# Performance work log

Hardware: AMD Instinct MI355X
Metric: run time of the kernel (lower is better)

Reference implementation:

```python
import jax, jax.numpy as jnp
import numpy as np

DIM = 1536
HEADS = 12
HD = DIM // HEADS  # 128
F, H, W = 4, 22, 40
L = F * H * W      # 3520
B = 1
EPS = 1e-6
SCALE = 1.0 / (HD ** 0.5)


def _rope_angles(max_pos=1024, head_dim=HD):
    # Wan rope_params: three blocks for (F,H,W) axes, dims (d-4*(d//6), 2*(d//6), 2*(d//6))
    d6 = head_dim // 6
    dims = [head_dim - 4 * d6, 2 * d6, 2 * d6]  # 44, 42, 42
    parts = []
    pos = np.arange(max_pos, dtype=np.float64)
    for dp in dims:
        inv = 1.0 / (10000.0 ** (np.arange(0, dp, 2, dtype=np.float64) / dp))
        parts.append(np.outer(pos, inv))  # [1024, dp//2]
    return np.concatenate(parts, axis=1).astype(np.float32)  # [1024, 64]


def setup_inputs() -> dict:
    key = jax.random.key(0)
    ks = jax.random.split(key, 10)
    std = 0.02
    inp = {
        "x": jax.random.normal(ks[0], (B, L, DIM), jnp.float32),
        "seq_lens": jnp.full((B,), L, jnp.int32),
        "grid_sizes": jnp.array([[F, H, W]], jnp.int32),
        "freqs": jnp.asarray(_rope_angles()),
        "Wq": jax.random.normal(ks[1], (DIM, DIM), jnp.float32) * std,
        "bq": jnp.zeros((DIM,), jnp.float32),
        "Wk": jax.random.normal(ks[2], (DIM, DIM), jnp.float32) * std,
        "bk": jnp.zeros((DIM,), jnp.float32),
        "Wv": jax.random.normal(ks[3], (DIM, DIM), jnp.float32) * std,
        "bv": jnp.zeros((DIM,), jnp.float32),
        "Wo": jax.random.normal(ks[4], (DIM, DIM), jnp.float32) * std,
        "bo": jnp.zeros((DIM,), jnp.float32),
        "gq": jnp.ones((DIM,), jnp.float32),
        "gk": jnp.ones((DIM,), jnp.float32),
    }
    return inp


def _rmsnorm(x, g):
    return x * jax.lax.rsqrt(jnp.mean(x * x, axis=-1, keepdims=True) + EPS) * g


def _rope_apply(x, grid_sizes, freqs):
    # x: [B, L, n, d]; freqs: [1024, d//2] angles. 3D grid RoPE (interleaved complex pairs).
    c = x.shape[-1] // 2  # 64
    sf = c - 2 * (c // 3)  # 22 freq channels for F axis; 21 each for H, W
    ff, fh, fw = freqs[:, :sf], freqs[:, sf:sf + c // 3], freqs[:, sf + c // 3:]

    def per_sample(xb, g):  # xb: [L, n, d], g: [3]
        f, h, w = g[0], g[1], g[2]
        idx = jnp.arange(xb.shape[0])
        fi = idx // (h * w)
        hi = (idx // w) % h
        wi = idx % w
        ang = jnp.concatenate([ff[fi], fh[hi], fw[wi]], axis=-1)  # [L, c]
        cos = jnp.cos(ang)[:, None, :]
        sin = jnp.sin(ang)[:, None, :]
        xr = xb.reshape(xb.shape[0], xb.shape[1], c, 2)
        x0, x1 = xr[..., 0], xr[..., 1]
        out = jnp.stack([x0 * cos - x1 * sin, x0 * sin + x1 * cos], axis=-1)
        return out.reshape(xb.shape)

    return jax.vmap(per_sample)(x, grid_sizes)


def reference(x, seq_lens, grid_sizes, freqs, Wq, bq, Wk, bk, Wv, bv, Wo, bo, gq, gk):
    b, s = x.shape[0], x.shape[1]
    q = _rmsnorm(x @ Wq.T + bq, gq).reshape(b, s, HEADS, HD)
    k = _rmsnorm(x @ Wk.T + bk, gk).reshape(b, s, HEADS, HD)
    v = (x @ Wv.T + bv).reshape(b, s, HEADS, HD)
    q = _rope_apply(q, grid_sizes, freqs)
    k = _rope_apply(k, grid_sizes, freqs)
    # non-causal full attention (seq_lens == L here, no padding mask needed)
    scores = jnp.einsum('bqnd,bknd->bnqk', q, k) * SCALE
    attn = jax.nn.softmax(scores, axis=-1)
    out = jnp.einsum('bnqk,bknd->bqnd', attn, v).reshape(b, s, DIM)
    return out @ Wo.T + bo
```

## Files before the change

kernel.cpp:

```cpp
#include <hip/hip_runtime.h>
#include <hip/hip_bf16.h>
#include <cstdint>

#define DIM   1536
#define HEADS 12
#define HD    128
#define LSEQ  3520
#define MPAD  3584
#define NKV   55
#define EPSF  1e-6f
#define QSCL  0.12751729198891580f

typedef __attribute__((ext_vector_type(4))) float f32x4;
typedef __attribute__((ext_vector_type(8))) short bf16x8;

__device__ __forceinline__ void gload16(const void* g, void* l) {
  __builtin_amdgcn_global_load_lds(
      (const __attribute__((address_space(1))) void*)g,
      (__attribute__((address_space(3))) void*)l, 16, 0, 0);
}

__device__ __forceinline__ ushort f2bf(float f) {
  union { float f; unsigned u; } v; v.f = f;
  unsigned u = v.u;
  return (ushort)((u + 0x7FFFu + ((u >> 16) & 1u)) >> 16);
}

__device__ __forceinline__ float bf2f(ushort u) {
  union { unsigned u; float f; } v; v.u = ((unsigned)u) << 16;
  return v.f;
}

#if __has_builtin(__builtin_amdgcn_exp2f)
__device__ __forceinline__ float ex2(float x) { return __builtin_amdgcn_exp2f(x); }
#else
__device__ __forceinline__ float ex2(float x) { return exp2f(x); }
#endif

__device__ __forceinline__ unsigned cvtpk(float a, float b) {
  unsigned r;
  asm("v_cvt_pk_bf16_f32 %0, %1, %2" : "=v"(r) : "v"(a), "v"(b));
  return r;
}

__global__ __launch_bounds__(256) void cast_all(const float* __restrict__ x,
    const float* __restrict__ Wq, const float* __restrict__ Wk,
    const float* __restrict__ Wv, const float* __restrict__ Wo,
    ushort* __restrict__ dst) {
  long e = ((long)blockIdx.x * 256 + threadIdx.x) * 8;
  const float* src;
  long off;
  if (e < (long)MPAD * DIM) {
    if (e >= (long)LSEQ * DIM) {
      *(bf16x8*)(dst + e) = (bf16x8)(short)0;
      return;
    }
    src = x; off = e;
  } else {
    long e2 = e - (long)MPAD * DIM;
    int wsel = (int)(e2 / ((long)DIM * DIM));
    off = e2 - (long)wsel * DIM * DIM;
    src = wsel == 0 ? Wq : (wsel == 1 ? Wk : (wsel == 2 ? Wv : Wo));
  }
  float4 a = *(const float4*)(src + off);
  float4 b = *(const float4*)(src + off + 4);
  bf16x8 o;
  o[0] = (short)f2bf(a.x); o[1] = (short)f2bf(a.y);
  o[2] = (short)f2bf(a.z); o[3] = (short)f2bf(a.w);
  o[4] = (short)f2bf(b.x); o[5] = (short)f2bf(b.y);
  o[6] = (short)f2bf(b.z); o[7] = (short)f2bf(b.w);
  *(bf16x8*)(dst + e) = o;
}

__global__ __launch_bounds__(256) void gemm_qkv(const ushort* __restrict__ A,
    const ushort* __restrict__ B3,
    const float* __restrict__ bq, const float* __restrict__ bk2, const float* __restrict__ bv2,
    ushort* __restrict__ qbb, ushort* __restrict__ kbb, ushort* __restrict__ vTt) {
  __shared__ ushort As[128 * 64];
  __shared__ ushort Bs[128 * 64];
  const int m0 = blockIdx.x * 128;
  const int n0g = blockIdx.y * 128;
  const int which = n0g / 1536;
  const int n0l = n0g - which * 1536;
  const int t = threadIdx.x;
  const int lane = t & 63;
  const int w = t >> 6;
  const int wr = w >> 1, wc = w & 1;
  const int sr = t >> 3;
  const int sc = t & 7;

  f32x4 acc[4][4];
#pragma unroll
  for (int i = 0; i < 4; ++i)
#pragma unroll
    for (int j = 0; j < 4; ++j) acc[i][j] = (f32x4)0.0f;

  const int arow = 64 * wr + (lane & 15);
  const int brow = 64 * wc + (lane & 15);

  for (int k0 = 0; k0 < DIM; k0 += 64) {
    __syncthreads();
#pragma unroll
    for (int i = 0; i < 4; ++i) {
      int row = sr + 32 * i;
      int cs = sc ^ (row & 7);
      gload16(A + (long)(m0 + row) * DIM + k0 + cs * 8, (char*)As + row * 128 + sc * 16);
      gload16(B3 + (long)(n0g + row) * DIM + k0 + cs * 8, (char*)Bs + row * 128 + sc * 16);
    }
    __syncthreads();
    bf16x8 af[4][2], bfr[4][2];
#pragma unroll
    for (int mi = 0; mi < 4; ++mi) {
      int row = arow + 16 * mi;
#pragma unroll
      for (int ks = 0; ks < 2; ++ks) {
        int ck = (ks * 4 + (lane >> 4)) ^ (row & 7);
        af[mi][ks] = *(const bf16x8*)(As + row * 64 + ck * 8);
      }
    }
#pragma unroll
    for (int ni = 0; ni < 4; ++ni) {
      int row = brow + 16 * ni;
#pragma unroll
      for (int ks = 0; ks < 2; ++ks) {
        int ck = (ks * 4 + (lane >> 4)) ^ (row & 7);
        bfr[ni][ks] = *(const bf16x8*)(Bs + row * 64 + ck * 8);
      }
    }
#pragma unroll
    for (int mi = 0; mi < 4; ++mi)
#pragma unroll
      for (int ni = 0; ni < 4; ++ni)
#pragma unroll
        for (int ks = 0; ks < 2; ++ks)
          acc[mi][ni] = __builtin_amdgcn_mfma_f32_16x16x32_bf16(
              af[mi][ks], bfr[ni][ks], acc[mi][ni], 0, 0, 0);
  }

  const float* bias = which == 0 ? bq : (which == 1 ? bk2 : bv2);
#pragma unroll
  for (int mi = 0; mi < 4; ++mi) {
#pragma unroll
    for (int ni = 0; ni < 4; ++ni) {
      int gmb = m0 + 64 * wr + 16 * mi + (lane >> 4) * 4;
      int gnl = n0l + 64 * wc + 16 * ni + (lane & 15);
      float bvv = bias[gnl];
      if (which == 2) {
        if (gmb < LSEQ) {
          ushort4 o;
          o.x = f2bf(acc[mi][ni][0] + bvv);
          o.y = f2bf(acc[mi][ni][1] + bvv);
          o.z = f2bf(acc[mi][ni][2] + bvv);
          o.w = f2bf(acc[mi][ni][3] + bvv);
          *(ushort4*)(vTt + (long)gnl * LSEQ + gmb) = o;
        }
      } else {
        ushort* dst = which ? kbb : qbb;
        if (gmb < LSEQ) {
#pragma unroll
          for (int j = 0; j < 4; ++j)
            dst[(long)(gmb + j) * DIM + gnl] = f2bf(acc[mi][ni][j] + bvv);
        }
      }
    }
  }
}

__global__ __launch_bounds__(256) void gemm_out(const ushort* __restrict__ A,
    const ushort* __restrict__ B, const float* __restrict__ bias,
    float* __restrict__ Cf) {
  __shared__ ushort As[128 * 64];
  __shared__ ushort Bs[128 * 64];
  const int m0 = blockIdx.x * 128;
  const int n0 = blockIdx.y * 128;
  const int t = threadIdx.x;
  const int lane = t & 63;
  const int w = t >> 6;
  const int wr = w >> 1, wc = w & 1;
  const int sr = t >> 3;
  const int sc = t & 7;

  f32x4 acc[4][4];
#pragma unroll
  for (int i = 0; i < 4; ++i)
#pragma unroll
    for (int j = 0; j < 4; ++j) acc[i][j] = (f32x4)0.0f;

  const int arow = 64 * wr + (lane & 15);
  const int brow = 64 * wc + (lane & 15);

  for (int k0 = 0; k0 < DIM; k0 += 64) {
    __syncthreads();
#pragma unroll
    for (int i = 0; i < 4; ++i) {
      int row = sr + 32 * i;
      int cs = sc ^ (row & 7);
      gload16(A + (long)(m0 + row) * DIM + k0 + cs * 8, (char*)As + row * 128 + sc * 16);
      gload16(B + (long)(n0 + row) * DIM + k0 + cs * 8, (char*)Bs + row * 128 + sc * 16);
    }
    __syncthreads();
    bf16x8 af[4][2], bfr[4][2];
#pragma unroll
    for (int mi = 0; mi < 4; ++mi) {
      int row = arow + 16 * mi;
#pragma unroll
      for (int ks = 0; ks < 2; ++ks) {
        int ck = (ks * 4 + (lane >> 4)) ^ (row & 7);
        af[mi][ks] = *(const bf16x8*)(As + row * 64 + ck * 8);
      }
    }
#pragma unroll
    for (int ni = 0; ni < 4; ++ni) {
      int row = brow + 16 * ni;
#pragma unroll
      for (int ks = 0; ks < 2; ++ks) {
        int ck = (ks * 4 + (lane >> 4)) ^ (row & 7);
        bfr[ni][ks] = *(const bf16x8*)(Bs + row * 64 + ck * 8);
      }
    }
#pragma unroll
    for (int mi = 0; mi < 4; ++mi)
#pragma unroll
      for (int ni = 0; ni < 4; ++ni)
#pragma unroll
        for (int ks = 0; ks < 2; ++ks)
          acc[mi][ni] = __builtin_amdgcn_mfma_f32_16x16x32_bf16(
              af[mi][ks], bfr[ni][ks], acc[mi][ni], 0, 0, 0);
  }

#pragma unroll
  for (int mi = 0; mi < 4; ++mi) {
#pragma unroll
    for (int ni = 0; ni < 4; ++ni) {
      int gmb = m0 + 64 * wr + 16 * mi + (lane >> 4) * 4;
      int gn  = n0 + 64 * wc + 16 * ni + (lane & 15);
      float bvv = bias[gn];
      if (gmb < LSEQ) {
#pragma unroll
        for (int j = 0; j < 4; ++j)
          Cf[(long)(gmb + j) * DIM + gn] = acc[mi][ni][j] + bvv;
      }
    }
  }
}

__global__ __launch_bounds__(256) void postqk_kernel(ushort* __restrict__ qb,
    ushort* __restrict__ kb, const float* __restrict__ gq_,
    const float* __restrict__ gk_, const float* __restrict__ freqs) {
  const int l = blockIdx.x;
  const int t = threadIdx.x;
  ushort* buf      = blockIdx.y ? kb : qb;
  const float* g   = blockIdx.y ? gk_ : gq_;
  const float post = blockIdx.y ? 1.0f : QSCL;
  ushort* row = buf + (long)l * DIM + t * 6;
  float v[6];
  {
    ushort2 p0 = *(const ushort2*)(row);
    ushort2 p1 = *(const ushort2*)(row + 2);
    ushort2 p2 = *(const ushort2*)(row + 4);
    v[0] = bf2f(p0.x); v[1] = bf2f(p0.y); v[2] = bf2f(p1.x);
    v[3] = bf2f(p1.y); v[4] = bf2f(p2.x); v[5] = bf2f(p2.y);
  }
  float ss = v[0]*v[0] + v[1]*v[1] + v[2]*v[2] + v[3]*v[3] + v[4]*v[4] + v[5]*v[5];
#pragma unroll
  for (int off = 1; off < 64; off <<= 1) ss += __shfl_xor(ss, off);
  __shared__ float red[4];
  if ((t & 63) == 0) red[t >> 6] = ss;
  __syncthreads();
  float scale = rsqrtf((red[0] + red[1] + red[2] + red[3]) * (1.0f / DIM) + EPSF) * post;
  const int fi = l / (22 * 40);
  const int hi = (l / 40) % 22;
  const int wi = l % 40;
  ushort o[6];
#pragma unroll
  for (int ii = 0; ii < 3; ++ii) {
    int pg = t * 3 + ii;
    int c = pg & 63;
    int rsel = (c < 22) ? fi : ((c < 43) ? hi : wi);
    float ang = freqs[rsel * 64 + c];
    float sn, cs;
    __sincosf(ang, &sn, &cs);
    float x0 = v[2*ii]   * scale * g[t*6 + 2*ii];
    float x1 = v[2*ii+1] * scale * g[t*6 + 2*ii+1];
    o[2*ii]   = f2bf(x0 * cs - x1 * sn);
    o[2*ii+1] = f2bf(x0 * sn + x1 * cs);
  }
  *(ushort2*)(row)     = make_ushort2(o[0], o[1]);
  *(ushort2*)(row + 2) = make_ushort2(o[2], o[3]);
  *(ushort2*)(row + 4) = make_ushort2(o[4], o[5]);
}

__global__ __launch_bounds__(256) void attn_kernel(const ushort* __restrict__ qb,
    const ushort* __restrict__ kb, const ushort* __restrict__ vT,
    ushort* __restrict__ ab) {
  __shared__ ushort KV[2][2][8192];
  __shared__ ushort Ps[4][32 * 40];
  __shared__ float2 Msh[4][2][16];
  const int qt = blockIdx.x;
  const int h  = blockIdx.y;
  const int t = threadIdx.x;
  const int lane = t & 63;
  const int w = t >> 6;
  const int a = w >> 1;
  const int b = w & 1;
  const int q16 = lane & 15;
  const int hi = lane >> 4;

  auto stageKV = [&](int buf, int kv0) {
    int rr = t >> 4, ck = t & 15;
#pragma unroll
    for (int i = 0; i < 4; ++i) {
      int row = rr + 16 * i;
      int cs = ck ^ (row & 7);
      gload16(kb + (long)(kv0 + row) * DIM + h * HD + cs * 8,
              (char*)&KV[buf][0][0] + row * 256 + ck * 16);
    }
    int rv = t >> 3, cv = t & 7;
#pragma unroll
    for (int i = 0; i < 4; ++i) {
      int row = rv + 32 * i;
      int cs = cv ^ (row & 7);
      gload16(vT + (long)(h * HD + row) * LSEQ + kv0 + cs * 8,
              (char*)&KV[buf][1][0] + row * 128 + cv * 16);
    }
  };

  {
    int rr = t >> 4, ck = t & 15;
#pragma unroll
    for (int i = 0; i < 4; ++i) {
      int row = rr + 16 * i;
      int cs = ck ^ (row & 7);
      gload16(qb + (long)(qt * 64 + row) * DIM + h * HD + cs * 8,
              (char*)&KV[1][0][0] + row * 256 + ck * 16);
    }
  }
  stageKV(0, 0);
  asm volatile("s_waitcnt vmcnt(8)" ::: "memory");
  __builtin_amdgcn_s_barrier();

  bf16x8 aq[2][4];
#pragma unroll
  for (int qf = 0; qf < 2; ++qf) {
    int row = a * 32 + qf * 16 + q16;
#pragma unroll
    for (int ks = 0; ks < 4; ++ks) {
      int ck = (ks * 4 + hi) ^ (row & 7);
      aq[qf][ks] = *(const bf16x8*)((const char*)&KV[1][0][0] + row * 256 + ck * 16);
    }
  }
  asm volatile("s_waitcnt lgkmcnt(0)" ::: "memory");
  __builtin_amdgcn_s_barrier();

  f32x4 acc[8][2];
#pragma unroll
  for (int i = 0; i < 8; ++i) { acc[i][0] = (f32x4)0.0f; acc[i][1] = (f32x4)0.0f; }
  float m_r[2] = {-1e30f, -1e30f};
  float l_r[2] = {0.f, 0.f};
  ushort* Psw = &Ps[w][0];

  auto compute = [&](int buf) {
    const ushort* Ks = &KV[buf][0][0];
    const ushort* Vs = &KV[buf][1][0];
    f32x4 s[2][2];
    s[0][0] = (f32x4)0.0f; s[0][1] = (f32x4)0.0f;
    s[1][0] = (f32x4)0.0f; s[1][1] = (f32x4)0.0f;
    __builtin_amdgcn_s_setprio(1);
#pragma unroll
    for (int kf = 0; kf < 2; ++kf) {
      int krow = b * 32 + kf * 16 + q16;
#pragma unroll
      for (int ks = 0; ks < 4; ++ks) {
        int ck = (ks * 4 + hi) ^ (krow & 7);
        bf16x8 kk = *(const bf16x8*)(Ks + krow * 128 + ck * 8);
        s[kf][0] = __builtin_amdgcn_mfma_f32_16x16x32_bf16(kk, aq[0][ks], s[kf][0], 0, 0, 0);
        s[kf][1] = __builtin_amdgcn_mfma_f32_16x16x32_bf16(kk, aq[1][ks], s[kf][1], 0, 0, 0);
      }
    }
    __builtin_amdgcn_s_setprio(0);
    float mx[2];
#pragma unroll
    for (int qf = 0; qf < 2; ++qf) {
      float m01 = fmaxf(fmaxf(s[0][qf][0], s[0][qf][1]), s[0][qf][2]);
      m01 = fmaxf(fmaxf(m01, s[0][qf][3]), s[1][qf][0]);
      m01 = fmaxf(fmaxf(m01, s[1][qf][1]), s[1][qf][2]);
      m01 = fmaxf(m01, s[1][qf][3]);
      m01 = fmaxf(m01, __shfl_xor(m01, 16));
      mx[qf] = fmaxf(m01, __shfl_xor(m01, 32));
    }
    bool noskip = !__all((mx[0] <= m_r[0] + 8.0f) & (mx[1] <= m_r[1] + 8.0f));
    if (noskip) {
#pragma unroll
      for (int qf = 0; qf < 2; ++qf) {
        float mnew = fmaxf(m_r[qf], mx[qf]);
        float fj = ex2(m_r[qf] - mnew);
        l_r[qf] *= fj;
        m_r[qf] = mnew;
#pragma unroll
        for (int ni = 0; ni < 8; ++ni) acc[ni][qf] *= fj;
      }
    }
#pragma unroll
    for (int qf = 0; qf < 2; ++qf) {
      float rs = 0.0f;
#pragma unroll
      for (int kf = 0; kf < 2; ++kf) {
        float p0 = ex2(s[kf][qf][0] - m_r[qf]);
        float p1 = ex2(s[kf][qf][1] - m_r[qf]);
        float p2 = ex2(s[kf][qf][2] - m_r[qf]);
        float p3 = ex2(s[kf][qf][3] - m_r[qf]);
        rs += (p0 + p1) + (p2 + p3);
        uint2 u;
        u.x = cvtpk(p0, p1);
        u.y = cvtpk(p2, p3);
        *(uint2*)(&Psw[(qf * 16 + q16) * 40 + kf * 16 + hi * 4]) = u;
      }
      rs += __shfl_xor(rs, 16);
      rs += __shfl_xor(rs, 32);
      l_r[qf] += rs;
    }
    bf16x8 pf[2];
    pf[0] = *(const bf16x8*)(&Psw[(0 * 16 + q16) * 40 + hi * 8]);
    pf[1] = *(const bf16x8*)(&Psw[(1 * 16 + q16) * 40 + hi * 8]);
    __builtin_amdgcn_s_setprio(1);
#pragma unroll
    for (int ni = 0; ni < 8; ++ni) {
      int vrow = 16 * ni + q16;
      int ck = (4 * b + hi) ^ (vrow & 7);
      bf16x8 vv = *(const bf16x8*)(Vs + vrow * 64 + ck * 8);
      acc[ni][0] = __builtin_amdgcn_mfma_f32_16x16x32_bf16(vv, pf[0], acc[ni][0], 0, 0, 0);
      acc[ni][1] = __builtin_amdgcn_mfma_f32_16x16x32_bf16(vv, pf[1], acc[ni][1], 0, 0, 0);
    }
    __builtin_amdgcn_s_setprio(0);
  };

  for (int tt = 0; tt < NKV - 1; ++tt) {
    stageKV((tt + 1) & 1, (tt + 1) * 64);
    asm volatile("s_waitcnt vmcnt(8)" ::: "memory");
    __builtin_amdgcn_s_barrier();
    compute(tt & 1);
    __builtin_amdgcn_s_barrier();
  }
  asm volatile("s_waitcnt vmcnt(0)" ::: "memory");
  __builtin_amdgcn_s_barrier();
  compute((NKV - 1) & 1);

  __syncthreads();
  if (hi < 2) Msh[w][hi][q16] = make_float2(m_r[hi], l_r[hi]);
  __syncthreads();
  float invl[2], fown[2];
#pragma unroll
  for (int qf = 0; qf < 2; ++qf) {
    float2 pm = Msh[w ^ 1][qf][q16];
    float ms = fmaxf(m_r[qf], pm.x);
    fown[qf] = ex2(m_r[qf] - ms);
    float ls = l_r[qf] * fown[qf] + pm.y * ex2(pm.x - ms);
    invl[qf] = 1.0f / ls;
  }
#pragma unroll
  for (int ni = 0; ni < 8; ++ni) {
    acc[ni][0] *= fown[0];
    acc[ni][1] *= fown[1];
  }
  char* xch = (char*)&KV[0][0][0] + a * 17408 + lane * 272;
  if (b == 1) {
#pragma unroll
    for (int ni = 0; ni < 8; ++ni) {
      *(f32x4*)(xch + (ni * 2 + 0) * 16) = acc[ni][0];
      *(f32x4*)(xch + (ni * 2 + 1) * 16) = acc[ni][1];
    }
  }
  __syncthreads();
  if (b == 0) {
#pragma unroll
    for (int ni = 0; ni < 8; ++ni) {
#pragma unroll
      for (int qf = 0; qf < 2; ++qf) {
        f32x4 o = acc[ni][qf] + *(const f32x4*)(xch + (ni * 2 + qf) * 16);
        float il = invl[qf];
        uint2 pk;
        pk.x = cvtpk(o[0] * il, o[1] * il);
        pk.y = cvtpk(o[2] * il, o[3] * il);
        int qrow = qt * 64 + a * 32 + qf * 16 + q16;
        *(uint2*)(ab + (long)qrow * DIM + h * HD + 16 * ni + hi * 4) = pk;
      }
    }
  }
}

extern "C" void kernel_launch(void* const* d_in, const int* in_sizes, int n_in,
                              void* d_out, int out_size, void* d_ws, size_t ws_size,
                              hipStream_t stream) {
  const float* x     = (const float*)d_in[0];
  const float* freqs = (const float*)d_in[3];
  const float* Wq = (const float*)d_in[4];  const float* bq = (const float*)d_in[5];
  const float* Wk = (const float*)d_in[6];  const float* bk = (const float*)d_in[7];
  const float* Wv = (const float*)d_in[8];  const float* bv = (const float*)d_in[9];
  const float* Wo = (const float*)d_in[10]; const float* bo = (const float*)d_in[11];
  const float* gq = (const float*)d_in[12]; const float* gk = (const float*)d_in[13];

  char* ws = (char*)d_ws;
  size_t off = 0;
  auto alloc = [&](size_t bytes) -> char* {
    char* p = ws + off;
    off += (bytes + 255) & ~(size_t)255;
    return p;
  };
  ushort* xb   = (ushort*)alloc((size_t)MPAD * DIM * 2 + 4 * (size_t)DIM * DIM * 2);
  ushort* wall = xb + (size_t)MPAD * DIM;
  ushort* wob  = wall + 3 * (size_t)DIM * DIM;
  ushort* qbb = (ushort*)alloc((size_t)LSEQ * DIM * 2);
  ushort* kbb = (ushort*)alloc((size_t)LSEQ * DIM * 2);
  ushort* vT  = (ushort*)alloc((size_t)DIM * LSEQ * 2);
  ushort* ab  = (ushort*)alloc((size_t)MPAD * DIM * 2);

  const long tot8 = ((long)MPAD * DIM + 4L * DIM * DIM) / 8;
  cast_all<<<(int)(tot8 / 256), 256, 0, stream>>>(x, Wq, Wk, Wv, Wo, xb);

  gemm_qkv<<<dim3(MPAD / 128, 36), 256, 0, stream>>>(xb, wall, bq, bk, bv, qbb, kbb, vT);

  postqk_kernel<<<dim3(LSEQ, 2), 256, 0, stream>>>(qbb, kbb, gq, gk, freqs);

  attn_kernel<<<dim3(NKV, HEADS), 256, 0, stream>>>(qbb, kbb, vT, ab);

  gemm_out<<<dim3(MPAD / 128, DIM / 128), 256, 0, stream>>>(ab, wob, bo, (float*)d_out);
}
```

Baseline: 403.4 us.

## Load V directly into registers, halve attention LDS, remap blocks per XCD

Attention no longer stages V tiles through shared memory. Each wave loads its V fragments straight from global memory into registers, which halves the LDS footprint so launch_bounds can ask for 3 blocks per CU. Blocks are launched on a 1D grid and remapped so each XCD gets a contiguous range of (head, q-tile) work, aiming for better L2 reuse of K/V per head. The epilogue exchange buffer gets an XOR swizzle to cut bank conflicts. In exchange, V global loads are uncoalesced 16-byte gathers issued inside the loop, which adds register pressure and latency.

```diff
diff --git a/kernel.cpp b/kernel.cpp
--- a/kernel.cpp
+++ b/kernel.cpp
@@ -290,14 +290,17 @@
   *(ushort2*)(row + 4) = make_ushort2(o[4], o[5]);
 }
 
-__global__ __launch_bounds__(256) void attn_kernel(const ushort* __restrict__ qb,
+__global__ __launch_bounds__(256, 3) void attn_kernel(const ushort* __restrict__ qb,
     const ushort* __restrict__ kb, const ushort* __restrict__ vT,
     ushort* __restrict__ ab) {
-  __shared__ ushort KV[2][2][8192];
+  __shared__ ushort Kd[2][64 * 128];
   __shared__ ushort Ps[4][32 * 40];
   __shared__ float2 Msh[4][2][16];
-  const int qt = blockIdx.x;
-  const int h  = blockIdx.y;
+  const int d = blockIdx.x;
+  const int xcd = d & 7, idx = d >> 3;
+  const int wflat = (xcd < 4 ? xcd * 83 : 332 + (xcd - 4) * 82) + idx;
+  const int h  = wflat / 55;
+  const int qt = wflat - h * 55;
   const int t = threadIdx.x;
   const int lane = t & 63;
   const int w = t >> 6;
@@ -306,22 +309,14 @@
   const int q16 = lane & 15;
   const int hi = lane >> 4;
 
-  auto stageKV = [&](int buf, int kv0) {
+  auto stageK = [&](int buf, int kv0) {
     int rr = t >> 4, ck = t & 15;
 #pragma unroll
     for (int i = 0; i < 4; ++i) {
       int row = rr + 16 * i;
       int cs = ck ^ (row & 7);
       gload16(kb + (long)(kv0 + row) * DIM + h * HD + cs * 8,
-              (char*)&KV[buf][0][0] + row * 256 + ck * 16);
-    }
-    int rv = t >> 3, cv = t & 7;
-#pragma unroll
-    for (int i = 0; i < 4; ++i) {
-      int row = rv + 32 * i;
-      int cs = cv ^ (row & 7);
-      gload16(vT + (long)(h * HD + row) * LSEQ + kv0 + cs * 8,
-              (char*)&KV[buf][1][0] + row * 128 + cv * 16);
+              (char*)&Kd[buf][0] + row * 256 + ck * 16);
     }
   };
 
@@ -332,11 +327,11 @@
       int row = rr + 16 * i;
       int cs = ck ^ (row & 7);
       gload16(qb + (long)(qt * 64 + row) * DIM + h * HD + cs * 8,
-              (char*)&KV[1][0][0] + row * 256 + ck * 16);
-    }
-  }
-  stageKV(0, 0);
-  asm volatile("s_waitcnt vmcnt(8)" ::: "memory");
+              (char*)&Kd[1][0] + row * 256 + ck * 16);
+    }
+  }
+  stageK(0, 0);
+  asm volatile("s_waitcnt vmcnt(4)" ::: "memory");
   __builtin_amdgcn_s_barrier();
 
   bf16x8 aq[2][4];
@@ -346,10 +341,11 @@
 #pragma unroll
     for (int ks = 0; ks < 4; ++ks) {
       int ck = (ks * 4 + hi) ^ (row & 7);
-      aq[qf][ks] = *(const bf16x8*)((const char*)&KV[1][0][0] + row * 256 + ck * 16);
+      aq[qf][ks] = *(const bf16x8*)((const char*)&Kd[1][0] + row * 256 + ck * 16);
     }
   }
   asm volatile("s_waitcnt lgkmcnt(0)" ::: "memory");
+  __builtin_amdgcn_sched_barrier(0);
   __builtin_amdgcn_s_barrier();
 
   f32x4 acc[8][2];
@@ -358,10 +354,18 @@
   float m_r[2] = {-1e30f, -1e30f};
   float l_r[2] = {0.f, 0.f};
   ushort* Psw = &Ps[w][0];
+  bf16x8 vv[8];
+
+  auto loadV = [&](int kv0) {
+#pragma unroll
+    for (int ni = 0; ni < 8; ++ni) {
+      int vrow = 16 * ni + q16;
+      vv[ni] = *(const bf16x8*)(vT + (long)(h * HD + vrow) * LSEQ + kv0 + b * 32 + hi * 8);
+    }
+  };
 
   auto compute = [&](int buf) {
-    const ushort* Ks = &KV[buf][0][0];
-    const ushort* Vs = &KV[buf][1][0];
+    const ushort* Ks = &Kd[buf][0];
     f32x4 s[2][2];
     s[0][0] = (f32x4)0.0f; s[0][1] = (f32x4)0.0f;
     s[1][0] = (f32x4)0.0f; s[1][1] = (f32x4)0.0f;
@@ -425,23 +429,22 @@
     __builtin_amdgcn_s_setprio(1);
 #pragma unroll
     for (int ni = 0; ni < 8; ++ni) {
-      int vrow = 16 * ni + q16;
-      int ck = (4 * b + hi) ^ (vrow & 7);
-      bf16x8 vv = *(const bf16x8*)(Vs + vrow * 64 + ck * 8);
-      acc[ni][0] = __builtin_amdgcn_mfma_f32_16x16x32_bf16(vv, pf[0], acc[ni][0], 0, 0, 0);
-      acc[ni][1] = __builtin_amdgcn_mfma_f32_16x16x32_bf16(vv, pf[1], acc[ni][1], 0, 0, 0);
+      acc[ni][0] = __builtin_amdgcn_mfma_f32_16x16x32_bf16(vv[ni], pf[0], acc[ni][0], 0, 0, 0);
+      acc[ni][1] = __builtin_amdgcn_mfma_f32_16x16x32_bf16(vv[ni], pf[1], acc[ni][1], 0, 0, 0);
     }
     __builtin_amdgcn_s_setprio(0);
   };
 
   for (int tt = 0; tt < NKV - 1; ++tt) {
-    stageKV((tt + 1) & 1, (tt + 1) * 64);
-    asm volatile("s_waitcnt vmcnt(8)" ::: "memory");
+    stageK((tt + 1) & 1, (tt + 1) * 64);
+    loadV(tt * 64);
+    asm volatile("s_waitcnt vmcnt(12)" ::: "memory");
     __builtin_amdgcn_s_barrier();
     compute(tt & 1);
     __builtin_amdgcn_s_barrier();
   }
-  asm volatile("s_waitcnt vmcnt(0)" ::: "memory");
+  loadV((NKV - 1) * 64);
+  asm volatile("s_waitcnt vmcnt(8)" ::: "memory");
   __builtin_amdgcn_s_barrier();
   compute((NKV - 1) & 1);
 
@@ -462,13 +465,13 @@
     acc[ni][0] *= fown[0];
     acc[ni][1] *= fown[1];
   }
-  char* xch = (char*)&KV[0][0][0] + a * 17408 + lane * 272;
+  char* xch = (char*)&Kd[0][0] + a * 16384 + lane * 256;
   if (b == 1) {
 #pragma unroll
-    for (int ni = 0; ni < 8; ++ni) {
-      *(f32x4*)(xch + (ni * 2 + 0) * 16) = acc[ni][0];
-      *(f32x4*)(xch + (ni * 2 + 1) * 16) = acc[ni][1];
-    }
+    for (int ni = 0; ni < 8; ++ni)
+#pragma unroll
+      for (int qf = 0; qf < 2; ++qf)
+        *(f32x4*)(xch + ((ni * 2 + qf) ^ (lane & 7)) * 16) = acc[ni][qf];
   }
   __syncthreads();
   if (b == 0) {
@@ -476,7 +479,7 @@
     for (int ni = 0; ni < 8; ++ni) {
 #pragma unroll
       for (int qf = 0; qf < 2; ++qf) {
-        f32x4 o = acc[ni][qf] + *(const f32x4*)(xch + (ni * 2 + qf) * 16);
+        f32x4 o = acc[ni][qf] + *(const f32x4*)(xch + ((ni * 2 + qf) ^ (lane & 7)) * 16);
         float il = invl[qf];
         uint2 pk;
         pk.x = cvtpk(o[0] * il, o[1] * il);
@@ -521,7 +524,7 @@
 
   postqk_kernel<<<dim3(LSEQ, 2), 256, 0, stream>>>(qbb, kbb, gq, gk, freqs);
 
-  attn_kernel<<<dim3(NKV, HEADS), 256, 0, stream>>>(qbb, kbb, vT, ab);
+  attn_kernel<<<NKV * HEADS, 256, 0, stream>>>(qbb, kbb, vT, ab);
 
   gemm_out<<<dim3(MPAD / 128, DIM / 128), 256, 0, stream>>>(ab, wob, bo, (float*)d_out);
 }
```

Result: slower. 541.9 us (+34.4%).

## Remap workgroup indices per XCD for L2 locality and swizzle attention exchange buffer

Applied to the files above, without the earlier changes.

Flattens the grids of the QKV GEMM, output GEMM and attention kernel, and remaps block IDs so that consecutive tiles (the same head, or neighbouring GEMM tiles) land on the same XCD, sharing that XCD's L2 for K/V and weight reuse. The attention partial-output exchange in LDS drops its padded stride in favour of an XOR swizzle to avoid bank conflicts. A sched_barrier is also added before the Q preload barrier. The mapping assumes round-robin dispatch of blocks across 8 XCDs and exact grid sizes, so it is hardcoded and brittle.

```diff
diff --git a/kernel.cpp b/kernel.cpp
--- a/kernel.cpp
+++ b/kernel.cpp
@@ -78,8 +78,11 @@
     ushort* __restrict__ qbb, ushort* __restrict__ kbb, ushort* __restrict__ vTt) {
   __shared__ ushort As[128 * 64];
   __shared__ ushort Bs[128 * 64];
-  const int m0 = blockIdx.x * 128;
-  const int n0g = blockIdx.y * 128;
+  const int dd = blockIdx.x;
+  const int f = (dd & 7) * 126 + (dd >> 3);
+  const int bx = f % 28, by = f / 28;
+  const int m0 = bx * 128;
+  const int n0g = by * 128;
   const int which = n0g / 1536;
   const int n0l = n0g - which * 1536;
   const int t = threadIdx.x;
@@ -171,8 +174,10 @@
     float* __restrict__ Cf) {
   __shared__ ushort As[128 * 64];
   __shared__ ushort Bs[128 * 64];
-  const int m0 = blockIdx.x * 128;
-  const int n0 = blockIdx.y * 128;
+  const int dd = blockIdx.x;
+  const int f = (dd & 7) * 42 + (dd >> 3);
+  const int m0 = (f % 28) * 128;
+  const int n0 = (f / 28) * 128;
   const int t = threadIdx.x;
   const int lane = t & 63;
   const int w = t >> 6;
@@ -296,8 +301,11 @@
   __shared__ ushort KV[2][2][8192];
   __shared__ ushort Ps[4][32 * 40];
   __shared__ float2 Msh[4][2][16];
-  const int qt = blockIdx.x;
-  const int h  = blockIdx.y;
+  const int d = blockIdx.x;
+  const int xcd = d & 7, idx = d >> 3;
+  const int wflat = (xcd < 4 ? xcd * 83 : 332 + (xcd - 4) * 82) + idx;
+  const int h  = wflat / 55;
+  const int qt = wflat - h * 55;
   const int t = threadIdx.x;
   const int lane = t & 63;
   const int w = t >> 6;
@@ -350,6 +358,7 @@
     }
   }
   asm volatile("s_waitcnt lgkmcnt(0)" ::: "memory");
+  __builtin_amdgcn_sched_barrier(0);
   __builtin_amdgcn_s_barrier();
 
   f32x4 acc[8][2];
@@ -462,13 +471,13 @@
     acc[ni][0] *= fown[0];
     acc[ni][1] *= fown[1];
   }
-  char* xch = (char*)&KV[0][0][0] + a * 17408 + lane * 272;
+  char* xch = (char*)&KV[0][0][0] + a * 16384 + lane * 256;
   if (b == 1) {
 #pragma unroll
-    for (int ni = 0; ni < 8; ++ni) {
-      *(f32x4*)(xch + (ni * 2 + 0) * 16) = acc[ni][0];
-      *(f32x4*)(xch + (ni * 2 + 1) * 16) = acc[ni][1];
-    }
+    for (int ni = 0; ni < 8; ++ni)
+#pragma unroll
+      for (int qf = 0; qf < 2; ++qf)
+        *(f32x4*)(xch + ((ni * 2 + qf) ^ (lane & 7)) * 16) = acc[ni][qf];
   }
   __syncthreads();
   if (b == 0) {
@@ -476,7 +485,7 @@
     for (int ni = 0; ni < 8; ++ni) {
 #pragma unroll
       for (int qf = 0; qf < 2; ++qf) {
-        f32x4 o = acc[ni][qf] + *(const f32x4*)(xch + (ni * 2 + qf) * 16);
+        f32x4 o = acc[ni][qf] + *(const f32x4*)(xch + ((ni * 2 + qf) ^ (lane & 7)) * 16);
         float il = invl[qf];
         uint2 pk;
         pk.x = cvtpk(o[0] * il, o[1] * il);
@@ -517,11 +526,11 @@
   const long tot8 = ((long)MPAD * DIM + 4L * DIM * DIM) / 8;
   cast_all<<<(int)(tot8 / 256), 256, 0, stream>>>(x, Wq, Wk, Wv, Wo, xb);
 
-  gemm_qkv<<<dim3(MPAD / 128, 36), 256, 0, stream>>>(xb, wall, bq, bk, bv, qbb, kbb, vT);
+  gemm_qkv<<<1008, 256, 0, stream>>>(xb, wall, bq, bk, bv, qbb, kbb, vT);
 
   postqk_kernel<<<dim3(LSEQ, 2), 256, 0, stream>>>(qbb, kbb, gq, gk, freqs);
 
-  attn_kernel<<<dim3(NKV, HEADS), 256, 0, stream>>>(qbb, kbb, vT, ab);
-
-  gemm_out<<<dim3(MPAD / 128, DIM / 128), 256, 0, stream>>>(ab, wob, bo, (float*)d_out);
-}
+  attn_kernel<<<NKV * HEADS, 256, 0, stream>>>(qbb, kbb, vT, ab);
+
+  gemm_out<<<336, 256, 0, stream>>>(ab, wob, bo, (float*)d_out);
+}
```

Result: no change. 404.5 us (+0.3%).
